# Performance work log

Hardware: AMD Instinct MI355X
Metric: run time of the kernel (lower is better)

The kernel has to match this reference:

```python
import jax, jax.numpy as jnp
import numpy as np

N_NODES = 10000
N_EDGES = 160000
N_FEATS = 9       # OGB atom features
VOCAB = 128       # >= max atom feature cardinality (119)
D = 128           # d_input == d_atom_emb
H = 4             # n_heads
C = 128           # out_channels per head (== d_input)
L = 3             # n_layers
N_CLASSES = 10
NEG_SLOPE = 0.2   # PyG GATConv default


def setup_inputs() -> dict:
    key = jax.random.key(0)
    ks = jax.random.split(key, 10)
    nodes_features = jax.random.randint(ks[0], (N_NODES, N_FEATS), 0, 119, dtype=jnp.int64)
    edges_connectivity = jax.random.randint(ks[1], (2, N_EDGES), 0, N_NODES, dtype=jnp.int64)
    s = 1.0 / np.sqrt(D)
    emb_tables = jax.random.normal(ks[2], (N_FEATS, VOCAB, D), dtype=jnp.float32) * s
    W = jax.random.normal(ks[3], (L, D, H * C), dtype=jnp.float32) * s
    att_src = jax.random.normal(ks[4], (L, H, C), dtype=jnp.float32) * s
    att_dst = jax.random.normal(ks[5], (L, H, C), dtype=jnp.float32) * s
    bias = jnp.zeros((L, C), dtype=jnp.float32)
    Wc = jax.random.normal(ks[6], (D, N_CLASSES), dtype=jnp.float32) * s
    bc = jnp.zeros((N_CLASSES,), dtype=jnp.float32)
    return {"nodes_features": nodes_features, "edges_connectivity": edges_connectivity,
            "emb_tables": emb_tables, "W": W, "att_src": att_src, "att_dst": att_dst,
            "bias": bias, "Wc": Wc, "bc": bc}


def _gat_layer(x, src, dst, W_l, a_s, a_d, b_l):
    # x: [N, D] -> h: [N, H, C]
    h = (x @ W_l).reshape(-1, H, C)
    alpha_src = jnp.einsum('nhc,hc->nh', h, a_s)  # [N, H]
    alpha_dst = jnp.einsum('nhc,hc->nh', h, a_d)  # [N, H]
    e = alpha_src[src] + alpha_dst[dst]           # [E, H]
    e = jnp.where(e >= 0, e, NEG_SLOPE * e)       # LeakyReLU(0.2)
    # segment softmax over edges grouped by destination node
    m = jax.ops.segment_max(e, dst, num_segments=N_NODES)  # [N, H]
    ex = jnp.exp(e - m[dst])
    s = jax.ops.segment_sum(ex, dst, num_segments=N_NODES)  # [N, H]
    alpha = ex / (s[dst] + 1e-16)                 # [E, H]
    msg = h[src] * alpha[..., None]               # [E, H, C]
    out = jax.ops.segment_sum(msg, dst, num_segments=N_NODES)  # [N, H, C]
    return out.mean(axis=1) + b_l                 # concat=False: mean over heads


def reference(nodes_features, edges_connectivity, emb_tables, W, att_src, att_dst, bias, Wc, bc):
    # AtomEncoder: sum per-feature embeddings -> [N, D]
    x = emb_tables[jnp.arange(N_FEATS), nodes_features].sum(axis=1)
    src, dst = edges_connectivity[0], edges_connectivity[1]
    for i in range(L):
        # dropout treated as identity (eval-mode reference)
        x = _gat_layer(x, src, dst, W[i], att_src[i], att_dst[i], bias[i])
        if i < L - 1:
            x = jax.nn.gelu(x)
    pooled = x.mean(axis=0)                       # graph mean-pool over nodes -> [D]
    return pooled @ Wc + bc                       # [n_classes]
```

## Files before the change

### kernel.cpp

```cpp
#include <hip/hip_runtime.h>
#include <hip/hip_bf16.h>
#include <math.h>

#define NN 10000
#define NE 160000
#define NF 9
#define VOCAB 128
#define D 128
#define NH 4
#define C 128
#define HC 512
#define NCLS 10
#define NL 3

__global__ __launch_bounds__(128)
void atom_encoder(const int* __restrict__ feats, const float* __restrict__ emb,
                  float* __restrict__ x) {
    int n = blockIdx.x;
    int d = threadIdx.x;
    __shared__ int f[NF];
    if (threadIdx.x < NF) f[threadIdx.x] = feats[n * NF + threadIdx.x];
    __syncthreads();
    float acc = 0.f;
#pragma unroll
    for (int i = 0; i < NF; ++i)
        acc += emb[(i * VOCAB + f[i]) * D + d];
    x[n * D + d] = acc;
}

__global__ __launch_bounds__(256)
void hist(const int* __restrict__ dst, int* __restrict__ deg) {
    int e = blockIdx.x * 256 + threadIdx.x;
    if (e < NE) atomicAdd(&deg[dst[e]], 1);
}

#define SCAN_T 1024
#define SCAN_PER ((NN + SCAN_T - 1) / SCAN_T)
__global__ __launch_bounds__(SCAN_T)
void scan_deg(const int* __restrict__ deg, int* __restrict__ rowstart,
              int* __restrict__ cursor) {
    __shared__ int part[SCAN_T];
    int t = threadIdx.x;
    int base = t * SCAN_PER;
    int vals[SCAN_PER];
    int loc = 0;
#pragma unroll
    for (int i = 0; i < SCAN_PER; ++i) {
        int idx = base + i;
        int v = (idx < NN) ? deg[idx] : 0;
        vals[i] = v;
        loc += v;
    }
    part[t] = loc;
    __syncthreads();
    for (int off = 1; off < SCAN_T; off <<= 1) {
        int y = (t >= off) ? part[t - off] : 0;
        __syncthreads();
        part[t] += y;
        __syncthreads();
    }
    int run = part[t] - loc;
#pragma unroll
    for (int i = 0; i < SCAN_PER; ++i) {
        int idx = base + i;
        if (idx < NN) { rowstart[idx] = run; cursor[idx] = run; }
        run += vals[i];
    }
}

__global__ __launch_bounds__(256)
void scatter(const int* __restrict__ src, const int* __restrict__ dst,
             int* __restrict__ cursor, int* __restrict__ csr_src) {
    int e = blockIdx.x * 256 + threadIdx.x;
    if (e < NE) {
        int p = atomicAdd(&cursor[dst[e]], 1);
        csr_src[p] = src[e];
    }
}

__global__ __launch_bounds__(128)
void prep_att(const float* __restrict__ W, const float* __restrict__ as_,
              const float* __restrict__ ad_, float* __restrict__ wsrc,
              float* __restrict__ wdst) {
    int l = blockIdx.x >> 3;
    int r = blockIdx.x & 7;
    int h = r >> 1;
    int side = r & 1;
    int k = threadIdx.x;
    const float* av = (side ? ad_ : as_) + (size_t)(l * NH + h) * C;
    const float* wrow = W + (size_t)l * D * HC + (size_t)k * HC + h * C;
    float acc = 0.f;
#pragma unroll 4
    for (int c = 0; c < C; ++c) acc += wrow[c] * av[c];
    float* o = (side ? wdst : wsrc) + (size_t)(l * NH + h) * D + k;
    *o = acc;
}

__global__ __launch_bounds__(256)
void alphas2(const float* __restrict__ X, const float* __restrict__ wsrc,
             const float* __restrict__ wdst, float* __restrict__ asrc,
             float* __restrict__ adst) {
    int n = blockIdx.x * 4 + (threadIdx.x >> 6);
    int lane = threadIdx.x & 63;
    float x0 = X[n * D + lane], x1 = X[n * D + lane + 64];
#pragma unroll
    for (int h = 0; h < NH; ++h) {
        float s = x0 * wsrc[h * D + lane] + x1 * wsrc[h * D + lane + 64];
        float d = x0 * wdst[h * D + lane] + x1 * wdst[h * D + lane + 64];
#pragma unroll
        for (int off = 32; off; off >>= 1) {
            s += __shfl_down(s, off);
            d += __shfl_down(d, off);
        }
        if (lane == 0) { asrc[n * NH + h] = s; adst[n * NH + h] = d; }
    }
}

__global__ __launch_bounds__(128)
void gat_agg(const int* __restrict__ csr_src, const int* __restrict__ rowstart,
             const int* __restrict__ degA, const float* __restrict__ asr,
             const float* __restrict__ adr, const float* __restrict__ X,
             float* __restrict__ agg) {
    int n = blockIdx.x;
    int t = threadIdx.x;
    int deg = degA[n];
    int start = rowstart[n];

    __shared__ float smax[NH];
    __shared__ float sinv[NH];
    __shared__ float lal[128][NH];
    __shared__ int lsrc[128];

    int h = t >> 5, i = t & 31;
    float ad_h = adr[n * NH + h];
    float mx = -INFINITY;
    for (int j = i; j < deg; j += 32) {
        int s = csr_src[start + j];
        float v = asr[s * NH + h] + ad_h;
        v = v >= 0.f ? v : 0.2f * v;
        mx = fmaxf(mx, v);
    }
#pragma unroll
    for (int off = 16; off; off >>= 1) mx = fmaxf(mx, __shfl_xor(mx, off));
    if (i == 0) smax[h] = mx;
    __syncthreads();
    float m = smax[h];
    float ss = 0.f;
    for (int j = i; j < deg; j += 32) {
        int s = csr_src[start + j];
        float v = asr[s * NH + h] + ad_h;
        v = v >= 0.f ? v : 0.2f * v;
        ss += __expf(v - m);
    }
#pragma unroll
    for (int off = 16; off; off >>= 1) ss += __shfl_xor(ss, off);
    if (i == 0) sinv[h] = 0.25f / (ss + 1e-16f);
    __syncthreads();

    float m0 = smax[0], m1 = smax[1], m2 = smax[2], m3 = smax[3];
    float i0 = sinv[0], i1 = sinv[1], i2 = sinv[2], i3 = sinv[3];
    float a0 = adr[n * NH + 0], a1 = adr[n * NH + 1];
    float a2 = adr[n * NH + 2], a3 = adr[n * NH + 3];
    float acc0 = 0.f, acc1 = 0.f, acc2 = 0.f, acc3 = 0.f;

    for (int cb = 0; cb < deg; cb += 128) {
        int cl = deg - cb; if (cl > 128) cl = 128;
        if (t < cl) {
            int s = csr_src[start + cb + t];
            float4 av = *(const float4*)(asr + s * NH);
            float v0 = av.x + a0; v0 = v0 >= 0.f ? v0 : 0.2f * v0;
            float v1 = av.y + a1; v1 = v1 >= 0.f ? v1 : 0.2f * v1;
            float v2 = av.z + a2; v2 = v2 >= 0.f ? v2 : 0.2f * v2;
            float v3 = av.w + a3; v3 = v3 >= 0.f ? v3 : 0.2f * v3;
            lal[t][0] = __expf(v0 - m0) * i0;
            lal[t][1] = __expf(v1 - m1) * i1;
            lal[t][2] = __expf(v2 - m2) * i2;
            lal[t][3] = __expf(v3 - m3) * i3;
            lsrc[t] = s;
        }
        __syncthreads();
#pragma unroll 4
        for (int j = 0; j < cl; ++j) {
            float xv = X[(size_t)lsrc[j] * D + t];
            float4 w = *(const float4*)lal[j];
            acc0 += w.x * xv;
            acc1 += w.y * xv;
            acc2 += w.z * xv;
            acc3 += w.w * xv;
        }
        __syncthreads();
    }

    float* o = agg + (size_t)n * HC + t;
    o[0 * D] = acc0;
    o[1 * D] = acc1;
    o[2 * D] = acc2;
    o[3 * D] = acc3;
}

#define BM 64
#define BN 64
#define BK 32
__global__ __launch_bounds__(256)
void gemm_out(const float* __restrict__ A, const float* __restrict__ Wm,
              const float* __restrict__ bias, float* __restrict__ Out,
              int do_gelu) {
    __shared__ float sA[BK][BM];
    __shared__ float sB[BK][BN];
    int t = threadIdx.x;
    int bm = blockIdx.x * BM;
    int bn = blockIdx.y * BN;
    int tr = t >> 4, tc = t & 15;
    float acc[4][4] = {};
    for (int kk = 0; kk < HC; kk += BK) {
#pragma unroll
        for (int i = 0; i < 2; ++i) {
            int j = t + i * 256;
            int row = j >> 3, kc = (j & 7) * 4;
            float4 v = make_float4(0.f, 0.f, 0.f, 0.f);
            int gr = bm + row;
            if (gr < NN) v = *(const float4*)(A + (size_t)gr * HC + kk + kc);
            sA[kc + 0][row] = v.x; sA[kc + 1][row] = v.y;
            sA[kc + 2][row] = v.z; sA[kc + 3][row] = v.w;
        }
#pragma unroll
        for (int i = 0; i < 2; ++i) {
            int jj = t + i * 256;
            int kr = jj >> 4, cc = (jj & 15) * 4;
            int j = kk + kr;
            *(float4*)&sB[kr][cc] =
                *(const float4*)(Wm + (size_t)(j & 127) * HC + (j >> 7) * C + bn + cc);
        }
        __syncthreads();
#pragma unroll
        for (int k = 0; k < BK; ++k) {
            float4 a = *(const float4*)&sA[k][tr * 4];
            float4 b = *(const float4*)&sB[k][tc * 4];
            float av[4] = {a.x, a.y, a.z, a.w};
            float bv[4] = {b.x, b.y, b.z, b.w};
#pragma unroll
            for (int mi = 0; mi < 4; ++mi)
#pragma unroll
                for (int ni = 0; ni < 4; ++ni)
                    acc[mi][ni] = fmaf(av[mi], bv[ni], acc[mi][ni]);
        }
        __syncthreads();
    }
#pragma unroll
    for (int mi = 0; mi < 4; ++mi) {
        int gr = bm + tr * 4 + mi;
        if (gr >= NN) continue;
        float4 r;
        float* rp = &r.x;
#pragma unroll
        for (int ni = 0; ni < 4; ++ni) {
            float v = acc[mi][ni] + bias[bn + tc * 4 + ni];
            if (do_gelu) {
                float u = 0.7978845608028654f * (v + 0.044715f * v * v * v);
                v = 0.5f * v * (1.f + tanhf(u));
            }
            rp[ni] = v;
        }
        *(float4*)(Out + (size_t)gr * D + bn + tc * 4) = r;
    }
}

__global__ __launch_bounds__(128)
void pool(const float* __restrict__ x, float* __restrict__ pooled) {
    int c = threadIdx.x;
    int chunk = (NN + gridDim.x - 1) / gridDim.x;
    int n0 = blockIdx.x * chunk;
    int n1 = n0 + chunk; if (n1 > NN) n1 = NN;
    float acc = 0.f;
    for (int n = n0; n < n1; ++n) acc += x[n * D + c];
    atomicAdd(pooled + c, acc);
}

__global__ __launch_bounds__(640)
void classify(const float* __restrict__ pooled, const float* __restrict__ Wc,
              const float* __restrict__ bc, float* __restrict__ out) {
    int k = threadIdx.x >> 6;
    int lane = threadIdx.x & 63;
    float acc = 0.f;
    for (int d = lane; d < D; d += 64)
        acc += pooled[d] * (1.0f / NN) * Wc[d * NCLS + k];
#pragma unroll
    for (int off = 32; off; off >>= 1) acc += __shfl_down(acc, off);
    if (lane == 0) out[k] = acc + bc[k];
}

extern "C" void kernel_launch(void* const* d_in, const int* in_sizes, int n_in,
                              void* d_out, int out_size, void* d_ws, size_t ws_size,
                              hipStream_t stream) {
    const int*   feats = (const int*)d_in[0];
    const int*   edges = (const int*)d_in[1];
    const float* emb   = (const float*)d_in[2];
    const float* W     = (const float*)d_in[3];
    const float* asrcW = (const float*)d_in[4];
    const float* adstW = (const float*)d_in[5];
    const float* bias  = (const float*)d_in[6];
    const float* Wc    = (const float*)d_in[7];
    const float* bc    = (const float*)d_in[8];
    float* out = (float*)d_out;

    const int* srcp = edges;
    const int* dstp = edges + NE;

    char* ws = (char*)d_ws;
    size_t off = 0;
    float* aggb   = (float*)(ws + off); off += (size_t)NN * HC * 4;
    float* xb0    = (float*)(ws + off); off += (size_t)NN * D * 4;
    float* xb1    = (float*)(ws + off); off += (size_t)NN * D * 4;
    float* asrc   = (float*)(ws + off); off += (size_t)NN * NH * 4;
    float* adst   = (float*)(ws + off); off += (size_t)NN * NH * 4;
    int*   deg    = (int*)(ws + off);   off += (size_t)NN * 4;
    int*   rowst  = (int*)(ws + off);   off += (size_t)NN * 4;
    int*   cursor = (int*)(ws + off);   off += (size_t)NN * 4;
    int*   csrsrc = (int*)(ws + off);   off += (size_t)NE * 4;
    float* wsrcb  = (float*)(ws + off); off += (size_t)NL * NH * D * 4;
    float* wdstb  = (float*)(ws + off); off += (size_t)NL * NH * D * 4;
    float* pooled = (float*)(ws + off); off += D * 4;

    hipMemsetAsync(deg, 0, (size_t)NN * 4, stream);
    hist<<<(NE + 255) / 256, 256, 0, stream>>>(dstp, deg);
    scan_deg<<<1, SCAN_T, 0, stream>>>(deg, rowst, cursor);
    scatter<<<(NE + 255) / 256, 256, 0, stream>>>(srcp, dstp, cursor, csrsrc);
    prep_att<<<NL * NH * 2, 128, 0, stream>>>(W, asrcW, adstW, wsrcb, wdstb);

    atom_encoder<<<NN, 128, 0, stream>>>(feats, emb, xb0);

    float* xin = xb0;
    float* xout = xb1;
    for (int l = 0; l < NL; ++l) {
        alphas2<<<NN / 4, 256, 0, stream>>>(xin, wsrcb + (size_t)l * NH * D,
                                            wdstb + (size_t)l * NH * D, asrc, adst);
        gat_agg<<<NN, 128, 0, stream>>>(csrsrc, rowst, deg, asrc, adst, xin, aggb);
        gemm_out<<<dim3((NN + BM - 1) / BM, D / BN), 256, 0, stream>>>(
            aggb, W + (size_t)l * D * HC, bias + (size_t)l * D, xout, l < 2 ? 1 : 0);
        float* tmp = xin; xin = xout; xout = tmp;
    }

    hipMemsetAsync(pooled, 0, D * 4, stream);
    pool<<<64, 128, 0, stream>>>(xin, pooled);
    classify<<<1, 640, 0, stream>>>(pooled, Wc, bc, out);
}
```

Before: 369.6 us.

## Use split-bf16 MFMA for output GEMM and fold last-layer GEMM into pooling

The fp32 FMA tiled GEMM is replaced by an MFMA bf16 kernel. Precision is kept by splitting the aggregated features and the weights into hi/lo bf16 parts and issuing three MFMAs per product. The last layer's GEMM is removed by exploiting linearity: the 512-wide aggregate is mean-pooled first, then multiplied by W3 in a small head kernel that also applies the classifier. gat_agg now writes bf16 hi/lo pairs, which halves per-element write size but needs two buffers, and the hi+lo sum drops the lo part's own low-order error.

```diff
diff --git a/kernel.cpp b/kernel.cpp
--- a/kernel.cpp
+++ b/kernel.cpp
@@ -12,6 +12,23 @@
 #define HC 512
 #define NCLS 10
 #define NL 3
+
+typedef __attribute__((ext_vector_type(8))) short bf16x8;
+typedef __attribute__((ext_vector_type(4))) float f32x4;
+
+__device__ __forceinline__ unsigned short f2bf(float f) {
+    unsigned u = __float_as_uint(f);
+    unsigned r = ((u >> 16) & 1u) + 0x7FFFu;
+    return (unsigned short)((u + r) >> 16);
+}
+__device__ __forceinline__ float bf2f(unsigned short h) {
+    return __uint_as_float(((unsigned)h) << 16);
+}
+__device__ __forceinline__ void fsplit(float v, unsigned short* hi, unsigned short* lo) {
+    unsigned short h = f2bf(v);
+    *hi = h;
+    *lo = f2bf(v - bf2f(h));
+}
 
 __global__ __launch_bounds__(128)
 void atom_encoder(const int* __restrict__ feats, const float* __restrict__ emb,
@@ -96,6 +113,20 @@
     *o = acc;
 }
 
+__global__ __launch_bounds__(512)
+void prep_w(const float* __restrict__ W, unsigned short* __restrict__ Bth,
+            unsigned short* __restrict__ Btl) {
+    int l = blockIdx.x >> 7;
+    int c = blockIdx.x & 127;
+    int j = threadIdx.x;
+    float v = W[(size_t)l * D * HC + (size_t)(j & 127) * HC + (j >> 7) * C + c];
+    unsigned short h, lo;
+    fsplit(v, &h, &lo);
+    size_t o = (size_t)(l * 128 + c) * HC + j;
+    Bth[o] = h;
+    Btl[o] = lo;
+}
+
 __global__ __launch_bounds__(256)
 void alphas2(const float* __restrict__ X, const float* __restrict__ wsrc,
              const float* __restrict__ wdst, float* __restrict__ asrc,
@@ -120,7 +151,7 @@
 void gat_agg(const int* __restrict__ csr_src, const int* __restrict__ rowstart,
              const int* __restrict__ degA, const float* __restrict__ asr,
              const float* __restrict__ adr, const float* __restrict__ X,
-             float* __restrict__ agg) {
+             unsigned short* __restrict__ aggh, unsigned short* __restrict__ aggl) {
     int n = blockIdx.x;
     int t = threadIdx.x;
     int deg = degA[n];
@@ -191,102 +222,114 @@
         __syncthreads();
     }
 
-    float* o = agg + (size_t)n * HC + t;
-    o[0 * D] = acc0;
-    o[1 * D] = acc1;
-    o[2 * D] = acc2;
-    o[3 * D] = acc3;
-}
-
-#define BM 64
-#define BN 64
-#define BK 32
-__global__ __launch_bounds__(256)
-void gemm_out(const float* __restrict__ A, const float* __restrict__ Wm,
-              const float* __restrict__ bias, float* __restrict__ Out,
-              int do_gelu) {
-    __shared__ float sA[BK][BM];
-    __shared__ float sB[BK][BN];
-    int t = threadIdx.x;
-    int bm = blockIdx.x * BM;
-    int bn = blockIdx.y * BN;
-    int tr = t >> 4, tc = t & 15;
-    float acc[4][4] = {};
-    for (int kk = 0; kk < HC; kk += BK) {
-#pragma unroll
-        for (int i = 0; i < 2; ++i) {
-            int j = t + i * 256;
-            int row = j >> 3, kc = (j & 7) * 4;
-            float4 v = make_float4(0.f, 0.f, 0.f, 0.f);
-            int gr = bm + row;
-            if (gr < NN) v = *(const float4*)(A + (size_t)gr * HC + kk + kc);
-            sA[kc + 0][row] = v.x; sA[kc + 1][row] = v.y;
-            sA[kc + 2][row] = v.z; sA[kc + 3][row] = v.w;
-        }
-#pragma unroll
-        for (int i = 0; i < 2; ++i) {
-            int jj = t + i * 256;
-            int kr = jj >> 4, cc = (jj & 15) * 4;
-            int j = kk + kr;
-            *(float4*)&sB[kr][cc] =
-                *(const float4*)(Wm + (size_t)(j & 127) * HC + (j >> 7) * C + bn + cc);
-        }
-        __syncthreads();
-#pragma unroll
-        for (int k = 0; k < BK; ++k) {
-            float4 a = *(const float4*)&sA[k][tr * 4];
-            float4 b = *(const float4*)&sB[k][tc * 4];
-            float av[4] = {a.x, a.y, a.z, a.w};
-            float bv[4] = {b.x, b.y, b.z, b.w};
-#pragma unroll
-            for (int mi = 0; mi < 4; ++mi)
-#pragma unroll
-                for (int ni = 0; ni < 4; ++ni)
-                    acc[mi][ni] = fmaf(av[mi], bv[ni], acc[mi][ni]);
-        }
-        __syncthreads();
-    }
-#pragma unroll
-    for (int mi = 0; mi < 4; ++mi) {
-        int gr = bm + tr * 4 + mi;
-        if (gr >= NN) continue;
-        float4 r;
-        float* rp = &r.x;
-#pragma unroll
-        for (int ni = 0; ni < 4; ++ni) {
-            float v = acc[mi][ni] + bias[bn + tc * 4 + ni];
+    size_t base = (size_t)n * HC + t;
+    unsigned short hh, ll;
+    fsplit(acc0, &hh, &ll); aggh[base + 0 * D] = hh; aggl[base + 0 * D] = ll;
+    fsplit(acc1, &hh, &ll); aggh[base + 1 * D] = hh; aggl[base + 1 * D] = ll;
+    fsplit(acc2, &hh, &ll); aggh[base + 2 * D] = hh; aggl[base + 2 * D] = ll;
+    fsplit(acc3, &hh, &ll); aggh[base + 3 * D] = hh; aggl[base + 3 * D] = ll;
+}
+
+__global__ __launch_bounds__(64)
+void gemm_mfma(const unsigned short* __restrict__ Ah, const unsigned short* __restrict__ Al,
+               const unsigned short* __restrict__ Bth, const unsigned short* __restrict__ Btl,
+               const float* __restrict__ bias, float* __restrict__ Out, int do_gelu) {
+    int lane = threadIdx.x;
+    int m0 = blockIdx.x * 16;
+    int n0 = blockIdx.y * 64;
+    int r = lane & 15;
+    int g = lane >> 4;
+
+    const bf16x8* ah = (const bf16x8*)(Ah + (size_t)(m0 + r) * HC + g * 8);
+    const bf16x8* al = (const bf16x8*)(Al + (size_t)(m0 + r) * HC + g * 8);
+    const bf16x8* bh0 = (const bf16x8*)(Bth + (size_t)(n0 + 0 * 16 + r) * HC + g * 8);
+    const bf16x8* bh1 = (const bf16x8*)(Bth + (size_t)(n0 + 1 * 16 + r) * HC + g * 8);
+    const bf16x8* bh2 = (const bf16x8*)(Bth + (size_t)(n0 + 2 * 16 + r) * HC + g * 8);
+    const bf16x8* bh3 = (const bf16x8*)(Bth + (size_t)(n0 + 3 * 16 + r) * HC + g * 8);
+    const bf16x8* bl0 = (const bf16x8*)(Btl + (size_t)(n0 + 0 * 16 + r) * HC + g * 8);
+    const bf16x8* bl1 = (const bf16x8*)(Btl + (size_t)(n0 + 1 * 16 + r) * HC + g * 8);
+    const bf16x8* bl2 = (const bf16x8*)(Btl + (size_t)(n0 + 2 * 16 + r) * HC + g * 8);
+    const bf16x8* bl3 = (const bf16x8*)(Btl + (size_t)(n0 + 3 * 16 + r) * HC + g * 8);
+
+    f32x4 acc[4];
+#pragma unroll
+    for (int q = 0; q < 4; ++q) acc[q] = (f32x4){0.f, 0.f, 0.f, 0.f};
+
+#pragma unroll 2
+    for (int ks = 0; ks < HC / 32; ++ks) {
+        bf16x8 a_h = ah[ks * 4];
+        bf16x8 a_l = al[ks * 4];
+        bf16x8 b;
+        b = bh0[ks * 4];
+        acc[0] = __builtin_amdgcn_mfma_f32_16x16x32_bf16(a_h, b, acc[0], 0, 0, 0);
+        acc[0] = __builtin_amdgcn_mfma_f32_16x16x32_bf16(a_l, b, acc[0], 0, 0, 0);
+        b = bl0[ks * 4];
+        acc[0] = __builtin_amdgcn_mfma_f32_16x16x32_bf16(a_h, b, acc[0], 0, 0, 0);
+        b = bh1[ks * 4];
+        acc[1] = __builtin_amdgcn_mfma_f32_16x16x32_bf16(a_h, b, acc[1], 0, 0, 0);
+        acc[1] = __builtin_amdgcn_mfma_f32_16x16x32_bf16(a_l, b, acc[1], 0, 0, 0);
+        b = bl1[ks * 4];
+        acc[1] = __builtin_amdgcn_mfma_f32_16x16x32_bf16(a_h, b, acc[1], 0, 0, 0);
+        b = bh2[ks * 4];
+        acc[2] = __builtin_amdgcn_mfma_f32_16x16x32_bf16(a_h, b, acc[2], 0, 0, 0);
+        acc[2] = __builtin_amdgcn_mfma_f32_16x16x32_bf16(a_l, b, acc[2], 0, 0, 0);
+        b = bl2[ks * 4];
+        acc[2] = __builtin_amdgcn_mfma_f32_16x16x32_bf16(a_h, b, acc[2], 0, 0, 0);
+        b = bh3[ks * 4];
+        acc[3] = __builtin_amdgcn_mfma_f32_16x16x32_bf16(a_h, b, acc[3], 0, 0, 0);
+        acc[3] = __builtin_amdgcn_mfma_f32_16x16x32_bf16(a_l, b, acc[3], 0, 0, 0);
+        b = bl3[ks * 4];
+        acc[3] = __builtin_amdgcn_mfma_f32_16x16x32_bf16(a_h, b, acc[3], 0, 0, 0);
+    }
+
+#pragma unroll
+    for (int q = 0; q < 4; ++q) {
+#pragma unroll
+        for (int i = 0; i < 4; ++i) {
+            int row = m0 + g * 4 + i;
+            int col = n0 + q * 16 + r;
+            float v = acc[q][i] + bias[col];
             if (do_gelu) {
                 float u = 0.7978845608028654f * (v + 0.044715f * v * v * v);
                 v = 0.5f * v * (1.f + tanhf(u));
             }
-            rp[ni] = v;
+            Out[(size_t)row * D + col] = v;
         }
-        *(float4*)(Out + (size_t)gr * D + bn + tc * 4) = r;
-    }
-}
-
-__global__ __launch_bounds__(128)
-void pool(const float* __restrict__ x, float* __restrict__ pooled) {
-    int c = threadIdx.x;
+    }
+}
+
+__global__ __launch_bounds__(512)
+void pool512(const unsigned short* __restrict__ Ah, const unsigned short* __restrict__ Al,
+             float* __restrict__ p) {
+    int t = threadIdx.x;
     int chunk = (NN + gridDim.x - 1) / gridDim.x;
     int n0 = blockIdx.x * chunk;
     int n1 = n0 + chunk; if (n1 > NN) n1 = NN;
     float acc = 0.f;
-    for (int n = n0; n < n1; ++n) acc += x[n * D + c];
-    atomicAdd(pooled + c, acc);
-}
-
-__global__ __launch_bounds__(640)
-void classify(const float* __restrict__ pooled, const float* __restrict__ Wc,
-              const float* __restrict__ bc, float* __restrict__ out) {
-    int k = threadIdx.x >> 6;
-    int lane = threadIdx.x & 63;
-    float acc = 0.f;
-    for (int d = lane; d < D; d += 64)
-        acc += pooled[d] * (1.0f / NN) * Wc[d * NCLS + k];
-#pragma unroll
-    for (int off = 32; off; off >>= 1) acc += __shfl_down(acc, off);
-    if (lane == 0) out[k] = acc + bc[k];
+    for (int n = n0; n < n1; ++n)
+        acc += bf2f(Ah[(size_t)n * HC + t]) + bf2f(Al[(size_t)n * HC + t]);
+    atomicAdd(p + t, acc);
+}
+
+__global__ __launch_bounds__(128)
+void final_head(const float* __restrict__ p512, const float* __restrict__ W3,
+                const float* __restrict__ bias3, const float* __restrict__ Wc,
+                const float* __restrict__ bc, float* __restrict__ out) {
+    __shared__ float t128[128];
+    int t = threadIdx.x;
+    float acc = bias3[t];
+    const float inv = 1.0f / NN;
+#pragma unroll 4
+    for (int j = 0; j < HC; ++j)
+        acc += p512[j] * inv * W3[(size_t)(j & 127) * HC + (j >> 7) * C + t];
+    t128[t] = acc;
+    __syncthreads();
+    if (t < NCLS) {
+        float o = bc[t];
+#pragma unroll 4
+        for (int c = 0; c < 128; ++c) o += t128[c] * Wc[c * NCLS + t];
+        out[t] = o;
+    }
 }
 
 extern "C" void kernel_launch(void* const* d_in, const int* in_sizes, int n_in,
@@ -308,7 +351,8 @@
 
     char* ws = (char*)d_ws;
     size_t off = 0;
-    float* aggb   = (float*)(ws + off); off += (size_t)NN * HC * 4;
+    unsigned short* aggh = (unsigned short*)(ws + off); off += (size_t)NN * HC * 2;
+    unsigned short* aggl = (unsigned short*)(ws + off); off += (size_t)NN * HC * 2;
     float* xb0    = (float*)(ws + off); off += (size_t)NN * D * 4;
     float* xb1    = (float*)(ws + off); off += (size_t)NN * D * 4;
     float* asrc   = (float*)(ws + off); off += (size_t)NN * NH * 4;
@@ -319,28 +363,36 @@
     int*   csrsrc = (int*)(ws + off);   off += (size_t)NE * 4;
     float* wsrcb  = (float*)(ws + off); off += (size_t)NL * NH * D * 4;
     float* wdstb  = (float*)(ws + off); off += (size_t)NL * NH * D * 4;
-    float* pooled = (float*)(ws + off); off += D * 4;
+    unsigned short* Bth = (unsigned short*)(ws + off); off += (size_t)2 * 128 * HC * 2;
+    unsigned short* Btl = (unsigned short*)(ws + off); off += (size_t)2 * 128 * HC * 2;
+    float* p512   = (float*)(ws + off); off += HC * 4;
 
     hipMemsetAsync(deg, 0, (size_t)NN * 4, stream);
     hist<<<(NE + 255) / 256, 256, 0, stream>>>(dstp, deg);
     scan_deg<<<1, SCAN_T, 0, stream>>>(deg, rowst, cursor);
     scatter<<<(NE + 255) / 256, 256, 0, stream>>>(srcp, dstp, cursor, csrsrc);
     prep_att<<<NL * NH * 2, 128, 0, stream>>>(W, asrcW, adstW, wsrcb, wdstb);
+    prep_w<<<2 * 128, 512, 0, stream>>>(W, Bth, Btl);
 
     atom_encoder<<<NN, 128, 0, stream>>>(feats, emb, xb0);
 
     float* xin = xb0;
     float* xout = xb1;
-    for (int l = 0; l < NL; ++l) {
+    for (int l = 0; l < 2; ++l) {
         alphas2<<<NN / 4, 256, 0, stream>>>(xin, wsrcb + (size_t)l * NH * D,
                                             wdstb + (size_t)l * NH * D, asrc, adst);
-        gat_agg<<<NN, 128, 0, stream>>>(csrsrc, rowst, deg, asrc, adst, xin, aggb);
-        gemm_out<<<dim3((NN + BM - 1) / BM, D / BN), 256, 0, stream>>>(
-            aggb, W + (size_t)l * D * HC, bias + (size_t)l * D, xout, l < 2 ? 1 : 0);
+        gat_agg<<<NN, 128, 0, stream>>>(csrsrc, rowst, deg, asrc, adst, xin, aggh, aggl);
+        gemm_mfma<<<dim3(NN / 16, 2), 64, 0, stream>>>(
+            aggh, aggl, Bth + (size_t)l * 128 * HC, Btl + (size_t)l * 128 * HC,
+            bias + (size_t)l * D, xout, 1);
         float* tmp = xin; xin = xout; xout = tmp;
     }
 
-    hipMemsetAsync(pooled, 0, D * 4, stream);
-    pool<<<64, 128, 0, stream>>>(xin, pooled);
-    classify<<<1, 640, 0, stream>>>(pooled, Wc, bc, out);
-}
+    alphas2<<<NN / 4, 256, 0, stream>>>(xin, wsrcb + (size_t)2 * NH * D,
+                                        wdstb + (size_t)2 * NH * D, asrc, adst);
+    gat_agg<<<NN, 128, 0, stream>>>(csrsrc, rowst, deg, asrc, adst, xin, aggh, aggl);
+    hipMemsetAsync(p512, 0, HC * 4, stream);
+    pool512<<<100, 512, 0, stream>>>(aggh, aggl, p512);
+    final_head<<<1, 128, 0, stream>>>(p512, W + (size_t)2 * D * HC,
+                                      bias + (size_t)2 * D, Wc, bc, out);
+}
```

After: 336.5 us. 1.1x faster.
